# Optimization experiments

Measured on AMD Instinct MI355X. Metric: run time of the kernel, lower is better.

## Reference

```python
import jax, jax.numpy as jnp
import numpy as np

DIM = 256
NUM_HEADS = 8
HEAD_DIM = DIM // NUM_HEADS


def setup_inputs() -> dict:
    key = jax.random.key(0)
    k_x, k_wq, k_bq, k_wp, k_bp = jax.random.split(key, 5)
    x = jax.random.normal(k_x, (4, DIM, 64, 64), dtype=jnp.float32)
    # 1x1 convs == per-pixel linear layers over channels
    w_qkv = jax.random.normal(k_wq, (3 * DIM, DIM), dtype=jnp.float32) * (DIM ** -0.5)
    b_qkv = jax.random.normal(k_bq, (3 * DIM,), dtype=jnp.float32) * 0.02
    w_proj = jax.random.normal(k_wp, (DIM, DIM), dtype=jnp.float32) * (DIM ** -0.5)
    b_proj = jax.random.normal(k_bp, (DIM,), dtype=jnp.float32) * 0.02
    return {"x": x, "w_qkv": w_qkv, "b_qkv": b_qkv, "w_proj": w_proj, "b_proj": b_proj}


def reference(x, w_qkv, b_qkv, w_proj, b_proj):
    B, C, H, W = x.shape
    S = H * W
    h, d = NUM_HEADS, HEAD_DIM
    # flatten spatial dims: (B, C, H, W) -> (B, S, C)
    xf = x.reshape(B, C, S).transpose(0, 2, 1)
    # 1x1 conv qkv: (B, S, 3C)
    qkv = xf @ w_qkv.T + b_qkv
    q, k, v = jnp.split(qkv, 3, axis=-1)
    # channel dim splits as (heads, head_dim): (B, S, C) -> (B, h, S, d)
    split = lambda t: t.reshape(B, S, h, d).transpose(0, 2, 1, 3)
    q, k, v = split(q), split(k), split(v)
    scale = d ** -0.5
    attn = jnp.einsum('bhsd,bhtd->bhst', q, k) * scale  # (B, h, S, S)
    attn = jax.nn.softmax(attn, axis=-1)
    out = jnp.einsum('bhst,bhtd->bhsd', attn, v)
    # merge heads: (B, h, S, d) -> (B, S, C)
    out = out.transpose(0, 2, 1, 3).reshape(B, S, C)
    out = out @ w_proj.T + b_proj
    # back to (B, C, H, W)
    return out.transpose(0, 2, 1).reshape(B, C, H, W)
```

## Files before the change

kernel.cpp:

```cpp
#include <hip/hip_runtime.h>


typedef __attribute__((ext_vector_type(8))) short short8;
typedef __attribute__((ext_vector_type(4))) float f4;

__device__ __forceinline__ short f2bs(float f) {
  union { float f; unsigned u; } v; v.f = f;
  unsigned r = v.u + 0x7FFFu + ((v.u >> 16) & 1u);
  return (short)(r >> 16);
}

__device__ __forceinline__ short8 cvt8(f4 a, f4 b) {
  short8 o;
  o[0] = f2bs(a[0]); o[1] = f2bs(a[1]); o[2] = f2bs(a[2]); o[3] = f2bs(a[3]);
  o[4] = f2bs(b[0]); o[5] = f2bs(b[1]); o[6] = f2bs(b[2]); o[7] = f2bs(b[3]);
  return o;
}

__global__ __launch_bounds__(256) void k_qkv(
    const float* __restrict__ x, const float* __restrict__ w,
    const float* __restrict__ bias,
    short* __restrict__ Qr, short* __restrict__ Kq, short* __restrict__ Vt) {
  const int tid = threadIdx.x;
  const int L = tid & 63, wv = tid >> 6;
  const int ln15 = L & 15, quad = L >> 4;
  const int mt = blockIdx.x;
  const int b = mt >> 6;
  const int s0 = (mt & 63) << 6;
  const int j0 = blockIdx.y << 6;
  const int jw = j0 + wv * 16;

  __shared__ __align__(16) short tl[4 * 64 * 16];

  f4 acc[4] = {{0,0,0,0},{0,0,0,0},{0,0,0,0},{0,0,0,0}};
  const float* wb = w + (jw + ln15) * 256 + quad * 8;
  const float* xb = x + b * (256 * 4096) + s0 + ln15;

#pragma unroll 2
  for (int cb = 0; cb < 256; cb += 32) {
    f4 a0 = *(const f4*)(wb + cb);
    f4 a1 = *(const f4*)(wb + cb + 4);
    short8 af = cvt8(a0, a1);
    const float* xc = xb + (cb + quad * 8) * 4096;
#pragma unroll
    for (int sub = 0; sub < 4; ++sub) {
      const float* xs = xc + sub * 16;
      short8 bf;
#pragma unroll
      for (int jj = 0; jj < 8; ++jj) bf[jj] = f2bs(xs[jj * 4096]);
      acc[sub] = __builtin_amdgcn_mfma_f32_16x16x32_bf16(af, bf, acc[sub], 0, 0, 0);
    }
  }

  float bj[4];
#pragma unroll
  for (int r = 0; r < 4; ++r) bj[r] = bias[jw + quad * 4 + r];

  const int type = j0 >> 8;
  if (type == 2) {
    const int jv = jw - 512;
    const int h = jv >> 5;
    const int dbase = jv & 31;
#pragma unroll
    for (int r = 0; r < 4; ++r) {
      const int d = dbase + quad * 4 + r;
      short* vp = Vt + (size_t)((b * 8 + h) * 32 + d) * 4096 + s0 + ln15;
#pragma unroll
      for (int sub = 0; sub < 4; ++sub)
        vp[sub * 16] = f2bs(acc[sub][r] + bj[r]);
    }
  } else {
    const float qsc = 0.17677669529663689f * 1.44269504088896f;
    const float mul = (type == 0) ? qsc : 1.0f;
    short* dst = (type == 0) ? Qr : Kq;
    const int hj = jw & 255;
    short* tw = tl + wv * 1024;
#pragma unroll
    for (int sub = 0; sub < 4; ++sub) {
      const int s = sub * 16 + ln15;
      const int swz = (s >> 2) & 1;
#pragma unroll
      for (int r = 0; r < 4; ++r) {
        const int dl = quad * 4 + r;
        tw[s * 16 + (((dl >> 3) ^ swz) * 8) + (dl & 7)] = f2bs((acc[sub][r] + bj[r]) * mul);
      }
    }
    const int h = hj >> 5;
    const int d0 = hj & 31;
#pragma unroll
    for (int i = 0; i < 2; ++i) {
      const int sl = i * 32 + (L >> 1);
      const int gg = L & 1;
      const int g2 = gg ^ ((sl >> 2) & 1);
      short8 row = *(const short8*)(tw + sl * 16 + g2 * 8);
      *(short8*)(dst + (size_t)((b * 8 + h) * 4096 + s0 + sl) * 32 + d0 + gg * 8) = row;
    }
  }
}

__global__ __launch_bounds__(256, 5) void k_attn(
    const short* __restrict__ Qr, const short* __restrict__ Kq,
    const short* __restrict__ Vt, short* __restrict__ O) {
  const int tid = threadIdx.x;
  const int L = tid & 63, wv = tid >> 6;
  const int ln15 = L & 15, quad = L >> 4;
  const int bh = blockIdx.y;
  const int b = bh >> 3, h = bh & 7;
  const int qt = wv & 1, half = wv >> 1;
  const int qb = blockIdx.x * 64 + qt * 32;

  const short* Qb = Qr + (size_t)bh * 4096 * 32;
  const short* Kb = Kq + (size_t)bh * 4096 * 32 + half * 2048 * 32;
  const short* Vb = Vt + (size_t)bh * 32 * 4096 + half * 2048;

  __shared__ float cbuf[2][32 * 33];
  __shared__ float l_up[2][32];

  short8 qf[2];
#pragma unroll
  for (int qs = 0; qs < 2; ++qs)
    qf[qs] = *(const short8*)(Qb + (qb + qs * 16 + ln15) * 32 + quad * 8);

  short8 ones;
#pragma unroll
  for (int j = 0; j < 8; ++j) ones[j] = (short)0x3F80;

  f4 acc[2][2] = {{{0,0,0,0},{0,0,0,0}},{{0,0,0,0},{0,0,0,0}}};
  f4 accl[2] = {{0,0,0,0},{0,0,0,0}};
  const f4 z4 = {0.f, 0.f, 0.f, 0.f};

  const short* kp = Kb + ln15 * 32 + quad * 8;
  const short* vp = Vb + ln15 * 4096 + quad * 8;

  for (int kb = 0; kb < 2048; kb += 64) {
    short8 vf[2][2];
#pragma unroll
    for (int f = 0; f < 2; ++f)
#pragma unroll
      for (int dg = 0; dg < 2; ++dg)
        vf[f][dg] = *(const short8*)(vp + dg * (16 * 4096) + kb + f * 32);

#pragma unroll
    for (int qs = 0; qs < 2; ++qs) {
      int dwa[4][2];
#pragma unroll
      for (int t = 0; t < 4; ++t) {
        short8 kf = *(const short8*)(kp + (kb + t * 16) * 32);
        f4 sc = __builtin_amdgcn_mfma_f32_16x16x32_bf16(kf, qf[qs], z4, 0, 0, 0);
        float p0 = __builtin_amdgcn_exp2f(sc[0]);
        float p1 = __builtin_amdgcn_exp2f(sc[1]);
        float p2 = __builtin_amdgcn_exp2f(sc[2]);
        float p3 = __builtin_amdgcn_exp2f(sc[3]);
        asm("v_cvt_pk_bf16_f32 %0, %1, %2" : "=v"(dwa[t][0]) : "v"(p0), "v"(p1));
        asm("v_cvt_pk_bf16_f32 %0, %1, %2" : "=v"(dwa[t][1]) : "v"(p2), "v"(p3));
      }
      union { int i[4]; short8 s; } pk[2];
#pragma unroll
      for (int f = 0; f < 2; ++f)
#pragma unroll
        for (int u = 0; u < 2; ++u) {
          int a = dwa[2 * f][u];
          int c = dwa[2 * f + 1][u];
          asm("v_permlane32_swap_b32 %0, %1" : "+v"(a), "+v"(c));
          asm("v_permlane16_swap_b32 %0, %1" : "+v"(a), "+v"(c));
          pk[f].i[u] = a;
          pk[f].i[u + 2] = c;
        }
      accl[qs] = __builtin_amdgcn_mfma_f32_16x16x32_bf16(pk[0].s, ones, accl[qs], 0, 0, 0);
      accl[qs] = __builtin_amdgcn_mfma_f32_16x16x32_bf16(pk[1].s, ones, accl[qs], 0, 0, 0);
      acc[qs][0] = __builtin_amdgcn_mfma_f32_16x16x32_bf16(pk[0].s, vf[0][0], acc[qs][0], 0, 0, 0);
      acc[qs][1] = __builtin_amdgcn_mfma_f32_16x16x32_bf16(pk[0].s, vf[0][1], acc[qs][1], 0, 0, 0);
      acc[qs][0] = __builtin_amdgcn_mfma_f32_16x16x32_bf16(pk[1].s, vf[1][0], acc[qs][0], 0, 0, 0);
      acc[qs][1] = __builtin_amdgcn_mfma_f32_16x16x32_bf16(pk[1].s, vf[1][1], acc[qs][1], 0, 0, 0);
    }
  }

  if (half == 1) {
    float* cw = cbuf[qt];
#pragma unroll
    for (int qs = 0; qs < 2; ++qs) {
#pragma unroll
      for (int dg = 0; dg < 2; ++dg)
#pragma unroll
        for (int r = 0; r < 4; ++r)
          cw[(qs * 16 + quad * 4 + r) * 33 + dg * 16 + ln15] = acc[qs][dg][r];
      if (ln15 == 0) {
#pragma unroll
        for (int r = 0; r < 4; ++r)
          l_up[qt][qs * 16 + quad * 4 + r] = accl[qs][r];
      }
    }
  }
  __syncthreads();
  if (half == 0) {
    const float* cu = cbuf[qt];
#pragma unroll
    for (int qs = 0; qs < 2; ++qs) {
#pragma unroll
      for (int r = 0; r < 4; ++r) {
        const float lup = l_up[qt][qs * 16 + quad * 4 + r];
        const float rl = 1.0f / (accl[qs][r] + lup);
        const int sg = qb + qs * 16 + quad * 4 + r;
        short* op = O + (size_t)(b * 4096 + sg) * 256 + h * 32 + ln15;
        const int ci = (qs * 16 + quad * 4 + r) * 33 + ln15;
        op[0]  = f2bs((acc[qs][0][r] + cu[ci]) * rl);
        op[16] = f2bs((acc[qs][1][r] + cu[ci + 16]) * rl);
      }
    }
  }
}

__global__ __launch_bounds__(256) void k_proj(
    const short* __restrict__ O, const float* __restrict__ w,
    const float* __restrict__ bias, float* __restrict__ out) {
  const int tid = threadIdx.x;
  const int L = tid & 63, wv = tid >> 6;
  const int ln15 = L & 15, quad = L >> 4;
  const int m0 = blockIdx.x * 64 + wv * 16;
  const int n0 = blockIdx.y << 6;
  const int b = m0 >> 12, s0 = m0 & 4095;

  f4 acc[4] = {{0,0,0,0},{0,0,0,0},{0,0,0,0},{0,0,0,0}};
  const short* Ob = O + (size_t)(m0 + ln15) * 256 + quad * 8;
  const float* wb = w + (n0 + ln15) * 256 + quad * 8;

#pragma unroll 2
  for (int cb = 0; cb < 256; cb += 32) {
    short8 af = *(const short8*)(Ob + cb);
#pragma unroll
    for (int sub = 0; sub < 4; ++sub) {
      f4 b0 = *(const f4*)(wb + sub * (16 * 256) + cb);
      f4 b1 = *(const f4*)(wb + sub * (16 * 256) + cb + 4);
      short8 bf = cvt8(b0, b1);
      acc[sub] = __builtin_amdgcn_mfma_f32_16x16x32_bf16(af, bf, acc[sub], 0, 0, 0);
    }
  }

  __shared__ float tl[4][64 * 17];
  float* tw = tl[wv];
#pragma unroll
  for (int sub = 0; sub < 4; ++sub) {
    const float bv = bias[n0 + sub * 16 + ln15];
#pragma unroll
    for (int r = 0; r < 4; ++r)
      tw[(sub * 16 + ln15) * 17 + quad * 4 + r] = acc[sub][r] + bv;
  }
#pragma unroll
  for (int i = 0; i < 4; ++i) {
    const int c = i * 16 + (L >> 2);
    const int ms = (L & 3) * 4;
    f4 v;
#pragma unroll
    for (int j = 0; j < 4; ++j) v[j] = tw[c * 17 + ms + j];
    *(f4*)(out + (size_t)b * (256 * 4096) + (size_t)(n0 + c) * 4096 + s0 + ms) = v;
  }
}

extern "C" void kernel_launch(void* const* d_in, const int* in_sizes, int n_in,
                              void* d_out, int out_size, void* d_ws, size_t ws_size,
                              hipStream_t stream) {
  const float* x      = (const float*)d_in[0];
  const float* w_qkv  = (const float*)d_in[1];
  const float* b_qkv  = (const float*)d_in[2];
  const float* w_proj = (const float*)d_in[3];
  const float* b_proj = (const float*)d_in[4];
  float* out = (float*)d_out;

  const size_t SEG = (size_t)4 * 8 * 4096 * 32;
  short* Qr = (short*)d_ws;
  short* Kq = Qr + SEG;
  short* Vt = Kq + SEG;
  short* O  = Vt + SEG;

  k_qkv <<<dim3(256, 12), 256, 0, stream>>>(x, w_qkv, b_qkv, Qr, Kq, Vt);
  k_attn<<<dim3(64, 32),  256, 0, stream>>>(Qr, Kq, Vt, O);
  k_proj<<<dim3(256, 4),  256, 0, stream>>>(O, w_proj, b_proj, out);
}
```

Before: 325.0 us.

## Double-buffer K fragments in registers and remap block indices across heads

```diff
diff --git a/kernel.cpp b/kernel.cpp
--- a/kernel.cpp
+++ b/kernel.cpp
@@ -104,10 +104,12 @@
   const int tid = threadIdx.x;
   const int L = tid & 63, wv = tid >> 6;
   const int ln15 = L & 15, quad = L >> 4;
-  const int bh = blockIdx.y;
+  const int p = blockIdx.y * 64 + blockIdx.x;
+  const int bh = (p & 7) * 4 + (p >> 9);
+  const int qblk = (p >> 3) & 63;
   const int b = bh >> 3, h = bh & 7;
   const int qt = wv & 1, half = wv >> 1;
-  const int qb = blockIdx.x * 64 + qt * 32;
+  const int qb = qblk * 64 + qt * 32;
 
   const short* Qb = Qr + (size_t)bh * 4096 * 32;
   const short* Kb = Kq + (size_t)bh * 4096 * 32 + half * 2048 * 32;
@@ -132,21 +134,26 @@
   const short* kp = Kb + ln15 * 32 + quad * 8;
   const short* vp = Vb + ln15 * 4096 + quad * 8;
 
-  for (int kb = 0; kb < 2048; kb += 64) {
-    short8 vf[2][2];
+  auto loadK = [&](int kb, short8* kr) {
+#pragma unroll
+    for (int t = 0; t < 4; ++t)
+      kr[t] = *(const short8*)(kp + (kb + t * 16) * 32);
+  };
+
+  auto chunk = [&](int kb, const short8* kr) {
+    short8 vf[4];
 #pragma unroll
     for (int f = 0; f < 2; ++f)
 #pragma unroll
       for (int dg = 0; dg < 2; ++dg)
-        vf[f][dg] = *(const short8*)(vp + dg * (16 * 4096) + kb + f * 32);
+        vf[f * 2 + dg] = *(const short8*)(vp + dg * (16 * 4096) + kb + f * 32);
 
 #pragma unroll
     for (int qs = 0; qs < 2; ++qs) {
       int dwa[4][2];
 #pragma unroll
       for (int t = 0; t < 4; ++t) {
-        short8 kf = *(const short8*)(kp + (kb + t * 16) * 32);
-        f4 sc = __builtin_amdgcn_mfma_f32_16x16x32_bf16(kf, qf[qs], z4, 0, 0, 0);
+        f4 sc = __builtin_amdgcn_mfma_f32_16x16x32_bf16(kr[t], qf[qs], z4, 0, 0, 0);
         float p0 = __builtin_amdgcn_exp2f(sc[0]);
         float p1 = __builtin_amdgcn_exp2f(sc[1]);
         float p2 = __builtin_amdgcn_exp2f(sc[2]);
@@ -168,12 +175,25 @@
         }
       accl[qs] = __builtin_amdgcn_mfma_f32_16x16x32_bf16(pk[0].s, ones, accl[qs], 0, 0, 0);
       accl[qs] = __builtin_amdgcn_mfma_f32_16x16x32_bf16(pk[1].s, ones, accl[qs], 0, 0, 0);
-      acc[qs][0] = __builtin_amdgcn_mfma_f32_16x16x32_bf16(pk[0].s, vf[0][0], acc[qs][0], 0, 0, 0);
-      acc[qs][1] = __builtin_amdgcn_mfma_f32_16x16x32_bf16(pk[0].s, vf[0][1], acc[qs][1], 0, 0, 0);
-      acc[qs][0] = __builtin_amdgcn_mfma_f32_16x16x32_bf16(pk[1].s, vf[1][0], acc[qs][0], 0, 0, 0);
-      acc[qs][1] = __builtin_amdgcn_mfma_f32_16x16x32_bf16(pk[1].s, vf[1][1], acc[qs][1], 0, 0, 0);
-    }
-  }
+      acc[qs][0] = __builtin_amdgcn_mfma_f32_16x16x32_bf16(pk[0].s, vf[0], acc[qs][0], 0, 0, 0);
+      acc[qs][1] = __builtin_amdgcn_mfma_f32_16x16x32_bf16(pk[0].s, vf[1], acc[qs][1], 0, 0, 0);
+      acc[qs][0] = __builtin_amdgcn_mfma_f32_16x16x32_bf16(pk[1].s, vf[2], acc[qs][0], 0, 0, 0);
+      acc[qs][1] = __builtin_amdgcn_mfma_f32_16x16x32_bf16(pk[1].s, vf[3], acc[qs][1], 0, 0, 0);
+    }
+  };
+
+  short8 kf0[4], kf1[4];
+  loadK(0, kf0);
+#pragma unroll 1
+  for (int kb = 0; kb < 1920; kb += 128) {
+    loadK(kb + 64, kf1);
+    chunk(kb, kf0);
+    loadK(kb + 128, kf0);
+    chunk(kb + 64, kf1);
+  }
+  loadK(1984, kf1);
+  chunk(1920, kf0);
+  chunk(1984, kf1);
 
   if (half == 1) {
     float* cw = cbuf[qt];
```

Result: slower. 332.6 us (+2.3%).

## Halve per-wave query tile in attention, double grid, remap blocks for locality

Applied to the files above, without the earlier changes.

```diff
diff --git a/kernel.cpp b/kernel.cpp
--- a/kernel.cpp
+++ b/kernel.cpp
@@ -98,114 +98,103 @@
   }
 }
 
-__global__ __launch_bounds__(256, 5) void k_attn(
+__global__ __launch_bounds__(256, 8) void k_attn(
     const short* __restrict__ Qr, const short* __restrict__ Kq,
     const short* __restrict__ Vt, short* __restrict__ O) {
   const int tid = threadIdx.x;
   const int L = tid & 63, wv = tid >> 6;
   const int ln15 = L & 15, quad = L >> 4;
-  const int bh = blockIdx.y;
+  const int p = blockIdx.y * 128 + blockIdx.x;
+  const int bh = (p & 7) * 4 + (p >> 10);
+  const int qblk = (p >> 3) & 127;
   const int b = bh >> 3, h = bh & 7;
   const int qt = wv & 1, half = wv >> 1;
-  const int qb = blockIdx.x * 64 + qt * 32;
+  const int qb = qblk * 32 + qt * 16;
 
   const short* Qb = Qr + (size_t)bh * 4096 * 32;
-  const short* Kb = Kq + (size_t)bh * 4096 * 32 + half * 2048 * 32;
+  const short* Kb = Kq + (size_t)bh * 4096 * 32 + half * (2048 * 32);
   const short* Vb = Vt + (size_t)bh * 32 * 4096 + half * 2048;
 
-  __shared__ float cbuf[2][32 * 33];
-  __shared__ float l_up[2][32];
-
-  short8 qf[2];
-#pragma unroll
-  for (int qs = 0; qs < 2; ++qs)
-    qf[qs] = *(const short8*)(Qb + (qb + qs * 16 + ln15) * 32 + quad * 8);
+  __shared__ float cbuf[2][16 * 33];
+  __shared__ float l_up[2][16];
+
+  short8 qf = *(const short8*)(Qb + (qb + ln15) * 32 + quad * 8);
 
   short8 ones;
 #pragma unroll
   for (int j = 0; j < 8; ++j) ones[j] = (short)0x3F80;
 
-  f4 acc[2][2] = {{{0,0,0,0},{0,0,0,0}},{{0,0,0,0},{0,0,0,0}}};
-  f4 accl[2] = {{0,0,0,0},{0,0,0,0}};
+  f4 acc[2] = {{0,0,0,0},{0,0,0,0}};
+  f4 accl = {0,0,0,0};
   const f4 z4 = {0.f, 0.f, 0.f, 0.f};
 
   const short* kp = Kb + ln15 * 32 + quad * 8;
   const short* vp = Vb + ln15 * 4096 + quad * 8;
 
+#pragma unroll 1
   for (int kb = 0; kb < 2048; kb += 64) {
-    short8 vf[2][2];
+    short8 kf[4];
+#pragma unroll
+    for (int t = 0; t < 4; ++t)
+      kf[t] = *(const short8*)(kp + (kb + t * 16) * 32);
+    int dwa[4][2];
+#pragma unroll
+    for (int t = 0; t < 4; ++t) {
+      f4 sc = __builtin_amdgcn_mfma_f32_16x16x32_bf16(kf[t], qf, z4, 0, 0, 0);
+      float p0 = __builtin_amdgcn_exp2f(sc[0]);
+      float p1 = __builtin_amdgcn_exp2f(sc[1]);
+      float p2 = __builtin_amdgcn_exp2f(sc[2]);
+      float p3 = __builtin_amdgcn_exp2f(sc[3]);
+      asm("v_cvt_pk_bf16_f32 %0, %1, %2" : "=v"(dwa[t][0]) : "v"(p0), "v"(p1));
+      asm("v_cvt_pk_bf16_f32 %0, %1, %2" : "=v"(dwa[t][1]) : "v"(p2), "v"(p3));
+    }
+    union { int i[4]; short8 s; } pk[2];
 #pragma unroll
     for (int f = 0; f < 2; ++f)
 #pragma unroll
-      for (int dg = 0; dg < 2; ++dg)
-        vf[f][dg] = *(const short8*)(vp + dg * (16 * 4096) + kb + f * 32);
-
-#pragma unroll
-    for (int qs = 0; qs < 2; ++qs) {
-      int dwa[4][2];
-#pragma unroll
-      for (int t = 0; t < 4; ++t) {
-        short8 kf = *(const short8*)(kp + (kb + t * 16) * 32);
-        f4 sc = __builtin_amdgcn_mfma_f32_16x16x32_bf16(kf, qf[qs], z4, 0, 0, 0);
-        float p0 = __builtin_amdgcn_exp2f(sc[0]);
-        float p1 = __builtin_amdgcn_exp2f(sc[1]);
-        float p2 = __builtin_amdgcn_exp2f(sc[2]);
-        float p3 = __builtin_amdgcn_exp2f(sc[3]);
-        asm("v_cvt_pk_bf16_f32 %0, %1, %2" : "=v"(dwa[t][0]) : "v"(p0), "v"(p1));
-        asm("v_cvt_pk_bf16_f32 %0, %1, %2" : "=v"(dwa[t][1]) : "v"(p2), "v"(p3));
+      for (int u = 0; u < 2; ++u) {
+        int a = dwa[2 * f][u];
+        int c = dwa[2 * f + 1][u];
+        asm("v_permlane32_swap_b32 %0, %1" : "+v"(a), "+v"(c));
+        asm("v_permlane16_swap_b32 %0, %1" : "+v"(a), "+v"(c));
+        pk[f].i[u] = a;
+        pk[f].i[u + 2] = c;
       }
-      union { int i[4]; short8 s; } pk[2];
-#pragma unroll
-      for (int f = 0; f < 2; ++f)
-#pragma unroll
-        for (int u = 0; u < 2; ++u) {
-          int a = dwa[2 * f][u];
-          int c = dwa[2 * f + 1][u];
-          asm("v_permlane32_swap_b32 %0, %1" : "+v"(a), "+v"(c));
-          asm("v_permlane16_swap_b32 %0, %1" : "+v"(a), "+v"(c));
-          pk[f].i[u] = a;
-          pk[f].i[u + 2] = c;
-        }
-      accl[qs] = __builtin_amdgcn_mfma_f32_16x16x32_bf16(pk[0].s, ones, accl[qs], 0, 0, 0);
-      accl[qs] = __builtin_amdgcn_mfma_f32_16x16x32_bf16(pk[1].s, ones, accl[qs], 0, 0, 0);
-      acc[qs][0] = __builtin_amdgcn_mfma_f32_16x16x32_bf16(pk[0].s, vf[0][0], acc[qs][0], 0, 0, 0);
-      acc[qs][1] = __builtin_amdgcn_mfma_f32_16x16x32_bf16(pk[0].s, vf[0][1], acc[qs][1], 0, 0, 0);
-      acc[qs][0] = __builtin_amdgcn_mfma_f32_16x16x32_bf16(pk[1].s, vf[1][0], acc[qs][0], 0, 0, 0);
-      acc[qs][1] = __builtin_amdgcn_mfma_f32_16x16x32_bf16(pk[1].s, vf[1][1], acc[qs][1], 0, 0, 0);
+    accl = __builtin_amdgcn_mfma_f32_16x16x32_bf16(pk[0].s, ones, accl, 0, 0, 0);
+    accl = __builtin_amdgcn_mfma_f32_16x16x32_bf16(pk[1].s, ones, accl, 0, 0, 0);
+#pragma unroll
+    for (int f = 0; f < 2; ++f) {
+      short8 vf0 = *(const short8*)(vp + kb + f * 32);
+      short8 vf1 = *(const short8*)(vp + 16 * 4096 + kb + f * 32);
+      acc[0] = __builtin_amdgcn_mfma_f32_16x16x32_bf16(pk[f].s, vf0, acc[0], 0, 0, 0);
+      acc[1] = __builtin_amdgcn_mfma_f32_16x16x32_bf16(pk[f].s, vf1, acc[1], 0, 0, 0);
     }
   }
 
   if (half == 1) {
     float* cw = cbuf[qt];
 #pragma unroll
-    for (int qs = 0; qs < 2; ++qs) {
-#pragma unroll
-      for (int dg = 0; dg < 2; ++dg)
-#pragma unroll
-        for (int r = 0; r < 4; ++r)
-          cw[(qs * 16 + quad * 4 + r) * 33 + dg * 16 + ln15] = acc[qs][dg][r];
-      if (ln15 == 0) {
-#pragma unroll
-        for (int r = 0; r < 4; ++r)
-          l_up[qt][qs * 16 + quad * 4 + r] = accl[qs][r];
-      }
+    for (int dg = 0; dg < 2; ++dg)
+#pragma unroll
+      for (int r = 0; r < 4; ++r)
+        cw[(quad * 4 + r) * 33 + dg * 16 + ln15] = acc[dg][r];
+    if (ln15 == 0) {
+#pragma unroll
+      for (int r = 0; r < 4; ++r)
+        l_up[qt][quad * 4 + r] = accl[r];
     }
   }
   __syncthreads();
   if (half == 0) {
     const float* cu = cbuf[qt];
 #pragma unroll
-    for (int qs = 0; qs < 2; ++qs) {
-#pragma unroll
-      for (int r = 0; r < 4; ++r) {
-        const float lup = l_up[qt][qs * 16 + quad * 4 + r];
-        const float rl = 1.0f / (accl[qs][r] + lup);
-        const int sg = qb + qs * 16 + quad * 4 + r;
-        short* op = O + (size_t)(b * 4096 + sg) * 256 + h * 32 + ln15;
-        const int ci = (qs * 16 + quad * 4 + r) * 33 + ln15;
-        op[0]  = f2bs((acc[qs][0][r] + cu[ci]) * rl);
-        op[16] = f2bs((acc[qs][1][r] + cu[ci + 16]) * rl);
-      }
+    for (int r = 0; r < 4; ++r) {
+      const float rl = 1.0f / (accl[r] + l_up[qt][quad * 4 + r]);
+      const int sg = qb + quad * 4 + r;
+      short* op = O + (size_t)(b * 4096 + sg) * 256 + h * 32 + ln15;
+      const int ci = (quad * 4 + r) * 33 + ln15;
+      op[0]  = f2bs((acc[0][r] + cu[ci]) * rl);
+      op[16] = f2bs((acc[1][r] + cu[ci + 16]) * rl);
     }
   }
 }
@@ -273,6 +262,6 @@
   short* O  = Vt + SEG;
 
   k_qkv <<<dim3(256, 12), 256, 0, stream>>>(x, w_qkv, b_qkv, Qr, Kq, Vt);
-  k_attn<<<dim3(64, 32),  256, 0, stream>>>(Qr, Kq, Vt, O);
+  k_attn<<<dim3(128, 32), 256, 0, stream>>>(Qr, Kq, Vt, O);
   k_proj<<<dim3(256, 4),  256, 0, stream>>>(O, w_proj, b_proj, out);
 }
```

Result: slower. 492.2 us (+51.5%).
